# Performance work log

Hardware: AMD Instinct MI355X
Metric: run time of the kernel (lower is better)

Reference implementation:

```python
import jax, jax.numpy as jnp
import numpy as np

V, E, H, L = 32000, 512, 512, 4
B, MAX_LEN = 32, 50
T = MAX_LEN + 1
SOS = 0
PAD_IDX = 2


def setup_inputs() -> dict:
    key = jax.random.key(0)
    ks = jax.random.split(key, 12)
    s = 1.0 / np.sqrt(H)  # pytorch LSTM default init scale
    emb = jax.random.uniform(ks[0], (V, E), minval=-0.1, maxval=0.1)
    emb = emb.at[PAD_IDX].set(0.0)  # padding_idx row zeroed
    inp = {
        "encoder_output": jax.random.normal(ks[1], (B, 50, E), dtype=jnp.float32),
        "decoder_hidden": jax.random.normal(ks[2], (L, B, H), dtype=jnp.float32),
        "decoder_cell": jax.random.normal(ks[3], (L, B, H), dtype=jnp.float32),
        "target_tensor": jax.random.randint(ks[4], (B, T), 0, V),
        "embedding": emb,
        # E == H so all layers stack into one [L, 4H, H] tensor
        "W_ih": jax.random.uniform(ks[5], (L, 4 * H, H), minval=-s, maxval=s),
        "W_hh": jax.random.uniform(ks[6], (L, 4 * H, H), minval=-s, maxval=s),
        "b_ih": jax.random.uniform(ks[7], (L, 4 * H), minval=-s, maxval=s),
        "b_hh": jax.random.uniform(ks[8], (L, 4 * H), minval=-s, maxval=s),
        "W_out": jax.random.uniform(ks[9], (V, H), minval=-0.1, maxval=0.1),
        "b_out": jnp.zeros((V,), dtype=jnp.float32),
    }
    return inp


def reference(encoder_output, decoder_hidden, decoder_cell, target_tensor,
              embedding, W_ih, W_hh, b_ih, b_hh, W_out, b_out):
    # teacher_forcing_ratio == 1 -> input at step 0 is SOS, step i is target[:, i-1]
    bsz = decoder_hidden.shape[1]
    sos = jnp.full((bsz, 1), SOS, dtype=target_tensor.dtype)
    tokens = jnp.concatenate([sos, target_tensor[:, : T - 1]], axis=1)  # [B, T]
    tokens_tb = tokens.T  # [T, B]

    def step(carry, tok):
        h, c = carry  # each [L, B, H]
        x = embedding[tok]  # [B, E]
        new_h, new_c = [], []
        for l in range(L):
            gates = x @ W_ih[l].T + b_ih[l] + h[l] @ W_hh[l].T + b_hh[l]  # [B, 4H]
            i, f, g, o = jnp.split(gates, 4, axis=-1)  # pytorch gate order i,f,g,o
            i, f, o = jax.nn.sigmoid(i), jax.nn.sigmoid(f), jax.nn.sigmoid(o)
            g = jnp.tanh(g)
            c_l = f * c[l] + i * g
            h_l = o * jnp.tanh(c_l)
            new_h.append(h_l)
            new_c.append(c_l)
            x = h_l  # input to next layer (dropout inactive in eval)
        # output projection uses PRE-clamp top-layer hidden (matches torch code)
        logits = x @ W_out.T + b_out  # [B, V]
        h = jnp.clip(jnp.stack(new_h), -50.0, 50.0)
        c = jnp.clip(jnp.stack(new_c), -50.0, 50.0)
        return (h, c), logits

    (h_fin, c_fin), logits_tbv = jax.lax.scan(step, (decoder_hidden, decoder_cell), tokens_tb)
    decoder_outputs = jnp.transpose(logits_tbv, (1, 0, 2))  # [B, T, V]
    return decoder_outputs, h_fin
```

## Files before the change

### kernel.cpp

```cpp
#include <hip/hip_runtime.h>

#define VSZ   32000
#define HSZ   512
#define LSZ   4
#define BSZ   32
#define TSZ   51
#define OUT_LOGITS 52224000
#define MPAD  1664

#define WS_XH    0
#define WS_HTOP  262144
#define WS_WB    688128
#define WS_CNT   8880128

typedef __attribute__((ext_vector_type(8))) short bf16x8;
typedef __attribute__((ext_vector_type(4))) float f32x4;

static __device__ __forceinline__ unsigned short f2bf(float f) {
    unsigned int u = __float_as_uint(f);
    unsigned int r = (u + 0x7FFFu + ((u >> 16) & 1u)) >> 16;
    return (unsigned short)r;
}

static __device__ __forceinline__ void split2(float f0, float f1,
                                              unsigned int& hi, unsigned int& lo) {
    unsigned int u0 = __float_as_uint(f0), u1 = __float_as_uint(f1);
    unsigned int h0 = u0 & 0xffff0000u, h1 = u1 & 0xffff0000u;
    hi = (u0 >> 16) | h1;
    float d0 = f0 - __uint_as_float(h0);
    float d1 = f1 - __uint_as_float(h1);
    lo = (__float_as_uint(d0) >> 16) | (__float_as_uint(d1) & 0xffff0000u);
}

static __device__ __forceinline__ void st_xh(float* p, float v) {
    __hip_atomic_store(p, v, __ATOMIC_RELAXED, __HIP_MEMORY_SCOPE_AGENT);
}
static __device__ __forceinline__ unsigned int ld_cnt(unsigned int* p) {
    return __hip_atomic_load(p, __ATOMIC_RELAXED, __HIP_MEMORY_SCOPE_AGENT);
}

__global__ __launch_bounds__(256) void convw_kernel(const float* __restrict__ W,
                                                    unsigned short* __restrict__ WB) {
    const int n4 = VSZ * HSZ / 4;
    for (int i = blockIdx.x * 256 + threadIdx.x; i < n4; i += gridDim.x * 256) {
        float4 f = ((const float4*)W)[i];
        ushort4 o;
        o.x = f2bf(f.x); o.y = f2bf(f.y); o.z = f2bf(f.z); o.w = f2bf(f.w);
        ((ushort4*)WB)[i] = o;
    }
}

__global__ __launch_bounds__(512, 2) void lstm_kernel(
    const float* __restrict__ dec_h, const float* __restrict__ dec_c,
    const int* __restrict__ target, const float* __restrict__ emb,
    const float* __restrict__ Wih, const float* __restrict__ Whh,
    const float* __restrict__ bih, const float* __restrict__ bhh,
    float* __restrict__ ws, float* __restrict__ out)
{
    __shared__ f32x4 red[4][64];

    float* XH = ws + WS_XH;
    unsigned short* HTOP = (unsigned short*)(ws + WS_HTOP);
    unsigned int* cnt = (unsigned int*)(ws + WS_CNT);

    const int tid  = threadIdx.x;
    const int lane = tid & 63;
    const int w    = tid >> 6;
    const int mt   = (w >> 1) & 1;
    const int nt   = w & 1;
    const int ks   = w >> 2;
    const int mi   = lane & 15;
    const int kg   = lane >> 4;
    const int l    = blockIdx.x >> 6;
    const int jt   = blockIdx.x & 63;

    const int jc = jt * 8 + mt * 4 + kg;
    const int bc = nt * 16 + mi;

    const int rjc = l * 2048 + jc;
    const float bias0 = bih[rjc]        + bhh[rjc];
    const float bias1 = bih[rjc + 512]  + bhh[rjc + 512];
    const float bias2 = bih[rjc + 1024] + bhh[rjc + 1024];
    const float bias3 = bih[rjc + 1536] + bhh[rjc + 1536];

    float c_reg = dec_c[(l * 32 + bc) * 512 + jc];

    bf16x8 wa_hi[16], wa_lo[16];
    {
        const int g_a   = mi & 3;
        const int jl_a  = mt * 4 + (mi >> 2);
        const int row_a = l * 2048 + g_a * 512 + jt * 8 + jl_a;
        const float* wrow = (ks ? Whh : Wih) + (size_t)row_a * 512;
        #pragma unroll
        for (int kk = 0; kk < 16; ++kk) {
            float4 v0 = *(const float4*)(wrow + kk * 32 + kg * 8);
            float4 v1 = *(const float4*)(wrow + kk * 32 + kg * 8 + 4);
            union { unsigned int u[4]; bf16x8 v; } H, L;
            split2(v0.x, v0.y, H.u[0], L.u[0]);
            split2(v0.z, v0.w, H.u[1], L.u[1]);
            split2(v1.x, v1.y, H.u[2], L.u[2]);
            split2(v1.z, v1.w, H.u[3], L.u[3]);
            wa_hi[kk] = H.v; wa_lo[kk] = L.v;
        }
    }

    {
        const int gid = blockIdx.x * 512 + tid;
        if (gid < 16384) {
            int k = gid >> 5, bb = gid & 31;
            st_xh(&XH[131072 + (k >> 2) * 128 + bb * 4 + (k & 3)], emb[k]);
        }
        if (gid < 65536) {
            int l2 = gid >> 14;
            int rem = gid & 16383;
            int j2 = rem >> 5, b2 = rem & 31;
            st_xh(&XH[((l2 + 1) & 1) * 131072 + l2 * 32768 +
                      (128 + (j2 >> 2)) * 128 + b2 * 4 + (j2 & 3)],
                  dec_h[(l2 * 32 + b2) * 512 + j2]);
        }
    }
    __syncthreads();
    if (tid == 0) {
        __builtin_amdgcn_fence(__ATOMIC_RELEASE, "agent");
        __hip_atomic_fetch_add(&cnt[256], 1u, __ATOMIC_RELAXED, __HIP_MEMORY_SCOPE_AGENT);
        while (ld_cnt(&cnt[256]) < 256u) { __builtin_amdgcn_s_sleep(1); }
        __builtin_amdgcn_fence(__ATOMIC_ACQUIRE, "agent");
    }
    __syncthreads();

    for (int s = 0; s < 54; ++s) {
        const int pp = (s + 1) & 1;
        const int pw = s & 1;
        const int t  = s - l;

        if (s > 0 && tid == 0) {
            while (ld_cnt(&cnt[l * 64 + s - 1]) < 64u) {}
            if (l > 0) while (ld_cnt(&cnt[(l - 1) * 64 + s - 1]) < 64u) {}
            if (l < 3) while (ld_cnt(&cnt[(l + 1) * 64 + s - 1]) < 64u) {}
            __builtin_amdgcn_fence(__ATOMIC_ACQUIRE, "agent");
        }
        __syncthreads();

        if (l == 0 && s < 50 && tid < 256) {
            int e = jt * 256 + tid;
            int k = e >> 5, bb = e & 31;
            int tok = target[bb * TSZ + s];
            st_xh(&XH[pw * 131072 + (k >> 2) * 128 + bb * 4 + (k & 3)],
                  emb[tok * 512 + k]);
        }

        if (t >= 0 && t <= 50) {
            const f32x4* xb4 = (const f32x4*)(XH + pp * 131072 + l * 32768)
                               + ks * 4096 + kg * 64 + bc;

            f32x4 acc_a = {0.f, 0.f, 0.f, 0.f};
            f32x4 acc_b = {0.f, 0.f, 0.f, 0.f};
            #pragma unroll
            for (int kk = 0; kk < 16; ++kk) {
                f32x4 x0 = xb4[kk * 256];
                f32x4 x1 = xb4[kk * 256 + 32];
                union { unsigned int u[4]; bf16x8 v; } XHI, XLO;
                split2(x0.x, x0.y, XHI.u[0], XLO.u[0]);
                split2(x0.z, x0.w, XHI.u[1], XLO.u[1]);
                split2(x1.x, x1.y, XHI.u[2], XLO.u[2]);
                split2(x1.z, x1.w, XHI.u[3], XLO.u[3]);
                acc_a = __builtin_amdgcn_mfma_f32_16x16x32_bf16(wa_hi[kk], XHI.v, acc_a, 0, 0, 0);
                acc_b = __builtin_amdgcn_mfma_f32_16x16x32_bf16(wa_lo[kk], XHI.v, acc_b, 0, 0, 0);
                acc_b = __builtin_amdgcn_mfma_f32_16x16x32_bf16(wa_hi[kk], XLO.v, acc_b, 0, 0, 0);
            }
            f32x4 acc = acc_a + acc_b;

            __syncthreads();
            if (w >= 4) red[w - 4][lane] = acc;
            __syncthreads();
            if (w < 4) {
                f32x4 rp = red[w][lane];
                float pi = acc[0] + rp[0] + bias0;
                float pf = acc[1] + rp[1] + bias1;
                float pg = acc[2] + rp[2] + bias2;
                float po = acc[3] + rp[3] + bias3;
                float ig = 1.f / (1.f + expf(-pi));
                float fg = 1.f / (1.f + expf(-pf));
                float gg = tanhf(pg);
                float og = 1.f / (1.f + expf(-po));
                float cn = fg * c_reg + ig * gg;
                float hn = og * tanhf(cn);
                c_reg     = fminf(fmaxf(cn, -50.f), 50.f);
                float hcl = fminf(fmaxf(hn, -50.f), 50.f);

                st_xh(&XH[pw * 131072 + l * 32768 + (128 + (jc >> 2)) * 128 + bc * 4 + (jc & 3)], hcl);
                if (l < 3)
                    st_xh(&XH[pw * 131072 + (l + 1) * 32768 + (jc >> 2) * 128 + bc * 4 + (jc & 3)], hn);
                if (l == 3)
                    HTOP[((t * 32 + bc) << 9) + jc] = f2bf(hn);
                if (t == 50)
                    out[OUT_LOGITS + ((l * 32 + bc) << 9) + jc] = hcl;
            }
        }

        __syncthreads();
        if (tid == 0) {
            __builtin_amdgcn_fence(__ATOMIC_RELEASE, "agent");
            __hip_atomic_fetch_add(&cnt[l * 64 + s], 1u, __ATOMIC_RELAXED,
                                   __HIP_MEMORY_SCOPE_AGENT);
        }
    }
}

__global__ __launch_bounds__(256) void proj_kernel(
    const unsigned short* __restrict__ A, const unsigned short* __restrict__ Bm,
    const float* __restrict__ bout, float* __restrict__ out)
{
    __shared__ unsigned short As[64 * 40];
    __shared__ unsigned short Bs[64 * 40];
    const int tid = threadIdx.x;
    const int bn = blockIdx.x;
    const int bm = blockIdx.y;
    const int w = tid >> 6, lane = tid & 63;
    const int lr = lane & 15, lq = lane >> 4;

    f32x4 acc0 = {0.f, 0.f, 0.f, 0.f};
    f32x4 acc1 = {0.f, 0.f, 0.f, 0.f};
    f32x4 acc2 = {0.f, 0.f, 0.f, 0.f};
    f32x4 acc3 = {0.f, 0.f, 0.f, 0.f};

    const int r = tid >> 2, c8 = (tid & 3) * 8;
    const unsigned short* Ag = A + (bm * 64 + r) * HSZ + c8;
    const unsigned short* Bg = Bm + (size_t)(bn * 64 + r) * HSZ + c8;

    for (int kt = 0; kt < 16; ++kt) {
        *(uint4*)&As[r * 40 + c8] = *(const uint4*)(Ag + kt * 32);
        *(uint4*)&Bs[r * 40 + c8] = *(const uint4*)(Bg + kt * 32);
        __syncthreads();
        bf16x8 af = *(const bf16x8*)&As[(w * 16 + lr) * 40 + lq * 8];
        bf16x8 b0 = *(const bf16x8*)&Bs[(0 * 16 + lr) * 40 + lq * 8];
        bf16x8 b1 = *(const bf16x8*)&Bs[(1 * 16 + lr) * 40 + lq * 8];
        bf16x8 b2 = *(const bf16x8*)&Bs[(2 * 16 + lr) * 40 + lq * 8];
        bf16x8 b3 = *(const bf16x8*)&Bs[(3 * 16 + lr) * 40 + lq * 8];
        acc0 = __builtin_amdgcn_mfma_f32_16x16x32_bf16(af, b0, acc0, 0, 0, 0);
        acc1 = __builtin_amdgcn_mfma_f32_16x16x32_bf16(af, b1, acc1, 0, 0, 0);
        acc2 = __builtin_amdgcn_mfma_f32_16x16x32_bf16(af, b2, acc2, 0, 0, 0);
        acc3 = __builtin_amdgcn_mfma_f32_16x16x32_bf16(af, b3, acc3, 0, 0, 0);
        __syncthreads();
    }

    f32x4 accs[4] = {acc0, acc1, acc2, acc3};
    #pragma unroll
    for (int nt = 0; nt < 4; ++nt) {
        const int v = bn * 64 + nt * 16 + lr;
        const float bo = bout[v];
        #pragma unroll
        for (int reg = 0; reg < 4; ++reg) {
            const int m = bm * 64 + w * 16 + lq * 4 + reg;
            if (m < TSZ * BSZ) {
                const int tt = m >> 5, bb = m & 31;
                out[(size_t)(bb * TSZ + tt) * VSZ + v] = accs[nt][reg] + bo;
            }
        }
    }
}

extern "C" void kernel_launch(void* const* d_in, const int* in_sizes, int n_in,
                              void* d_out, int out_size, void* d_ws, size_t ws_size,
                              hipStream_t stream) {
    const float* dec_h = (const float*)d_in[1];
    const float* dec_c = (const float*)d_in[2];
    const int*   tgt   = (const int*)d_in[3];
    const float* emb   = (const float*)d_in[4];
    const float* Wih   = (const float*)d_in[5];
    const float* Whh   = (const float*)d_in[6];
    const float* bihp  = (const float*)d_in[7];
    const float* bhhp  = (const float*)d_in[8];
    const float* Wout  = (const float*)d_in[9];
    const float* bout  = (const float*)d_in[10];
    float* out = (float*)d_out;
    float* ws  = (float*)d_ws;

    unsigned short* HTOP = (unsigned short*)(ws + WS_HTOP);
    unsigned short* WB   = (unsigned short*)(ws + WS_WB);

    hipMemsetAsync(ws + WS_CNT, 0, 1040, stream);

    convw_kernel<<<4096, 256, 0, stream>>>(Wout, WB);

    void* args[] = { (void*)&dec_h, (void*)&dec_c, (void*)&tgt, (void*)&emb,
                     (void*)&Wih, (void*)&Whh, (void*)&bihp, (void*)&bhhp,
                     (void*)&ws, (void*)&out };
    hipLaunchCooperativeKernel(reinterpret_cast<void*>(lstm_kernel),
                               dim3(256), dim3(512), args, 0, stream);

    proj_kernel<<<dim3(VSZ / 64, MPAD / 64), 256, 0, stream>>>(HTOP, WB, bout, out);
}
```

Baseline: 1.142 ms.

## Store LSTM state pre-split into bf16 hi/lo pairs to skip per-step splitting

```diff
diff --git a/kernel.cpp b/kernel.cpp
--- a/kernel.cpp
+++ b/kernel.cpp
@@ -32,12 +32,21 @@
     lo = (__float_as_uint(d0) >> 16) | (__float_as_uint(d1) & 0xffff0000u);
 }
 
-static __device__ __forceinline__ void st_xh(float* p, float v) {
-    __hip_atomic_store(p, v, __ATOMIC_RELAXED, __HIP_MEMORY_SCOPE_AGENT);
-}
 static __device__ __forceinline__ unsigned int ld_cnt(unsigned int* p) {
     return __hip_atomic_load(p, __ATOMIC_RELAXED, __HIP_MEMORY_SCOPE_AGENT);
 }
+
+static __device__ __forceinline__ void st_split(unsigned short* base, float v) {
+    unsigned int u = __float_as_uint(v);
+    unsigned int h = u & 0xffff0000u;
+    float d = v - __uint_as_float(h);
+    __hip_atomic_store(base, (unsigned short)(u >> 16),
+                       __ATOMIC_RELAXED, __HIP_MEMORY_SCOPE_AGENT);
+    __hip_atomic_store(base + 8, (unsigned short)(__float_as_uint(d) >> 16),
+                       __ATOMIC_RELAXED, __HIP_MEMORY_SCOPE_AGENT);
+}
+
+#define XHB_IDX(buf, layer, k8, b) (((((buf)*4 + (layer))*128 + (k8))*32 + (b))*16)
 
 __global__ __launch_bounds__(256) void convw_kernel(const float* __restrict__ W,
                                                     unsigned short* __restrict__ WB) {
@@ -59,7 +68,7 @@
 {
     __shared__ f32x4 red[4][64];
 
-    float* XH = ws + WS_XH;
+    unsigned short* XHB = (unsigned short*)(ws + WS_XH);
     unsigned short* HTOP = (unsigned short*)(ws + WS_HTOP);
     unsigned int* cnt = (unsigned int*)(ws + WS_CNT);
 
@@ -108,15 +117,14 @@
         const int gid = blockIdx.x * 512 + tid;
         if (gid < 16384) {
             int k = gid >> 5, bb = gid & 31;
-            st_xh(&XH[131072 + (k >> 2) * 128 + bb * 4 + (k & 3)], emb[k]);
+            st_split(XHB + XHB_IDX(1, 0, k >> 3, bb) + (k & 7), emb[k]);
         }
         if (gid < 65536) {
             int l2 = gid >> 14;
             int rem = gid & 16383;
             int j2 = rem >> 5, b2 = rem & 31;
-            st_xh(&XH[((l2 + 1) & 1) * 131072 + l2 * 32768 +
-                      (128 + (j2 >> 2)) * 128 + b2 * 4 + (j2 & 3)],
-                  dec_h[(l2 * 32 + b2) * 512 + j2]);
+            st_split(XHB + XHB_IDX((l2 + 1) & 1, l2, 64 + (j2 >> 3), b2) + (j2 & 7),
+                     dec_h[(l2 * 32 + b2) * 512 + j2]);
         }
     }
     __syncthreads();
@@ -134,9 +142,15 @@
         const int t  = s - l;
 
         if (s > 0 && tid == 0) {
-            while (ld_cnt(&cnt[l * 64 + s - 1]) < 64u) {}
-            if (l > 0) while (ld_cnt(&cnt[(l - 1) * 64 + s - 1]) < 64u) {}
-            if (l < 3) while (ld_cnt(&cnt[(l + 1) * 64 + s - 1]) < 64u) {}
+            unsigned int* c0 = &cnt[l * 64 + s - 1];
+            unsigned int* c1 = (l > 0) ? &cnt[(l - 1) * 64 + s - 1] : c0;
+            unsigned int* c2 = (l < 3) ? &cnt[(l + 1) * 64 + s - 1] : c0;
+            for (;;) {
+                unsigned int a = ld_cnt(c0);
+                unsigned int b2 = ld_cnt(c1);
+                unsigned int c3 = ld_cnt(c2);
+                if (a >= 64u && b2 >= 64u && c3 >= 64u) break;
+            }
             __builtin_amdgcn_fence(__ATOMIC_ACQUIRE, "agent");
         }
         __syncthreads();
@@ -145,32 +159,25 @@
             int e = jt * 256 + tid;
             int k = e >> 5, bb = e & 31;
             int tok = target[bb * TSZ + s];
-            st_xh(&XH[pw * 131072 + (k >> 2) * 128 + bb * 4 + (k & 3)],
-                  emb[tok * 512 + k]);
+            st_split(XHB + XHB_IDX(pw, 0, k >> 3, bb) + (k & 7),
+                     emb[tok * 512 + k]);
         }
 
         if (t >= 0 && t <= 50) {
-            const f32x4* xb4 = (const f32x4*)(XH + pp * 131072 + l * 32768)
-                               + ks * 4096 + kg * 64 + bc;
+            const unsigned short* xb = XHB + XHB_IDX(pp, l, ks * 64 + kg, bc);
 
             f32x4 acc_a = {0.f, 0.f, 0.f, 0.f};
             f32x4 acc_b = {0.f, 0.f, 0.f, 0.f};
             #pragma unroll
             for (int kk = 0; kk < 16; ++kk) {
-                f32x4 x0 = xb4[kk * 256];
-                f32x4 x1 = xb4[kk * 256 + 32];
-                union { unsigned int u[4]; bf16x8 v; } XHI, XLO;
-                split2(x0.x, x0.y, XHI.u[0], XLO.u[0]);
-                split2(x0.z, x0.w, XHI.u[1], XLO.u[1]);
-                split2(x1.x, x1.y, XHI.u[2], XLO.u[2]);
-                split2(x1.z, x1.w, XHI.u[3], XLO.u[3]);
-                acc_a = __builtin_amdgcn_mfma_f32_16x16x32_bf16(wa_hi[kk], XHI.v, acc_a, 0, 0, 0);
-                acc_b = __builtin_amdgcn_mfma_f32_16x16x32_bf16(wa_lo[kk], XHI.v, acc_b, 0, 0, 0);
-                acc_b = __builtin_amdgcn_mfma_f32_16x16x32_bf16(wa_hi[kk], XLO.v, acc_b, 0, 0, 0);
+                bf16x8 xhi = *(const bf16x8*)(xb + kk * 2048);
+                bf16x8 xlo = *(const bf16x8*)(xb + kk * 2048 + 8);
+                acc_a = __builtin_amdgcn_mfma_f32_16x16x32_bf16(wa_hi[kk], xhi, acc_a, 0, 0, 0);
+                acc_b = __builtin_amdgcn_mfma_f32_16x16x32_bf16(wa_lo[kk], xhi, acc_b, 0, 0, 0);
+                acc_b = __builtin_amdgcn_mfma_f32_16x16x32_bf16(wa_hi[kk], xlo, acc_b, 0, 0, 0);
             }
             f32x4 acc = acc_a + acc_b;
 
-            __syncthreads();
             if (w >= 4) red[w - 4][lane] = acc;
             __syncthreads();
             if (w < 4) {
@@ -188,9 +195,9 @@
                 c_reg     = fminf(fmaxf(cn, -50.f), 50.f);
                 float hcl = fminf(fmaxf(hn, -50.f), 50.f);
 
-                st_xh(&XH[pw * 131072 + l * 32768 + (128 + (jc >> 2)) * 128 + bc * 4 + (jc & 3)], hcl);
+                st_split(XHB + XHB_IDX(pw, l, 64 + (jc >> 3), bc) + (jc & 7), hcl);
                 if (l < 3)
-                    st_xh(&XH[pw * 131072 + (l + 1) * 32768 + (jc >> 2) * 128 + bc * 4 + (jc & 3)], hn);
+                    st_split(XHB + XHB_IDX(pw, l + 1, jc >> 3, bc) + (jc & 7), hn);
                 if (l == 3)
                     HTOP[((t * 32 + bc) << 9) + jc] = f2bf(hn);
                 if (t == 50)
```

New measurement: 1.330 ms. 16.5% more time.

## Quad-buffer LSTM state and precompute embeddings to relax inter-layer barriers

Applied to the files above, without the earlier changes.

```diff
diff --git a/kernel.cpp b/kernel.cpp
--- a/kernel.cpp
+++ b/kernel.cpp
@@ -9,9 +9,10 @@
 #define MPAD  1664
 
 #define WS_XH    0
-#define WS_HTOP  262144
-#define WS_WB    688128
-#define WS_CNT   8880128
+#define WS_X0    524288
+#define WS_HTOP  1359872
+#define WS_WB    1785856
+#define WS_CNT   9977856
 
 typedef __attribute__((ext_vector_type(8))) short bf16x8;
 typedef __attribute__((ext_vector_type(4))) float f32x4;
@@ -60,6 +61,7 @@
     __shared__ f32x4 red[4][64];
 
     float* XH = ws + WS_XH;
+    float* X0 = ws + WS_X0;
     unsigned short* HTOP = (unsigned short*)(ws + WS_HTOP);
     unsigned int* cnt = (unsigned int*)(ws + WS_CNT);
 
@@ -106,17 +108,21 @@
 
     {
         const int gid = blockIdx.x * 512 + tid;
-        if (gid < 16384) {
-            int k = gid >> 5, bb = gid & 31;
-            st_xh(&XH[131072 + (k >> 2) * 128 + bb * 4 + (k & 3)], emb[k]);
-        }
         if (gid < 65536) {
             int l2 = gid >> 14;
             int rem = gid & 16383;
             int j2 = rem >> 5, b2 = rem & 31;
-            st_xh(&XH[((l2 + 1) & 1) * 131072 + l2 * 32768 +
+            st_xh(&XH[((l2 + 3) & 3) * 131072 + l2 * 32768 +
                       (128 + (j2 >> 2)) * 128 + b2 * 4 + (j2 & 3)],
                   dec_h[(l2 * 32 + b2) * 512 + j2]);
+        }
+        for (int idx = gid; idx < TSZ * 16384; idx += 131072) {
+            int tt2 = idx >> 14;
+            int rem = idx & 16383;
+            int k = rem >> 5, bb = rem & 31;
+            int tok = tt2 ? target[bb * TSZ + tt2 - 1] : 0;
+            st_xh(&X0[tt2 * 16384 + (k >> 2) * 128 + bb * 4 + (k & 3)],
+                  emb[tok * 512 + k]);
         }
     }
     __syncthreads();
@@ -129,29 +135,29 @@
     __syncthreads();
 
     for (int s = 0; s < 54; ++s) {
-        const int pp = (s + 1) & 1;
-        const int pw = s & 1;
+        const int rp = (s + 3) & 3;
+        const int wp = s & 3;
         const int t  = s - l;
 
         if (s > 0 && tid == 0) {
-            while (ld_cnt(&cnt[l * 64 + s - 1]) < 64u) {}
-            if (l > 0) while (ld_cnt(&cnt[(l - 1) * 64 + s - 1]) < 64u) {}
-            if (l < 3) while (ld_cnt(&cnt[(l + 1) * 64 + s - 1]) < 64u) {}
+            unsigned int* c0 = &cnt[l * 64 + s - 1];
+            unsigned int* c1 = (l > 0) ? &cnt[(l - 1) * 64 + s - 1] : c0;
+            unsigned int* c2 = (l < 3 && s >= 3) ? &cnt[(l + 1) * 64 + s - 3] : c0;
+            for (;;) {
+                unsigned int a  = ld_cnt(c0);
+                unsigned int b2 = ld_cnt(c1);
+                unsigned int c3 = ld_cnt(c2);
+                if (a >= 64u && b2 >= 64u && c3 >= 64u) break;
+            }
             __builtin_amdgcn_fence(__ATOMIC_ACQUIRE, "agent");
         }
         __syncthreads();
 
-        if (l == 0 && s < 50 && tid < 256) {
-            int e = jt * 256 + tid;
-            int k = e >> 5, bb = e & 31;
-            int tok = target[bb * TSZ + s];
-            st_xh(&XH[pw * 131072 + (k >> 2) * 128 + bb * 4 + (k & 3)],
-                  emb[tok * 512 + k]);
-        }
-
         if (t >= 0 && t <= 50) {
-            const f32x4* xb4 = (const f32x4*)(XH + pp * 131072 + l * 32768)
-                               + ks * 4096 + kg * 64 + bc;
+            const float* xbase = (l == 0 && ks == 0)
+                               ? (X0 + t * 16384)
+                               : (XH + rp * 131072 + l * 32768 + ks * 16384);
+            const f32x4* xb4 = (const f32x4*)xbase + kg * 64 + bc;
 
             f32x4 acc_a = {0.f, 0.f, 0.f, 0.f};
             f32x4 acc_b = {0.f, 0.f, 0.f, 0.f};
@@ -170,15 +176,14 @@
             }
             f32x4 acc = acc_a + acc_b;
 
-            __syncthreads();
             if (w >= 4) red[w - 4][lane] = acc;
             __syncthreads();
             if (w < 4) {
-                f32x4 rp = red[w][lane];
-                float pi = acc[0] + rp[0] + bias0;
-                float pf = acc[1] + rp[1] + bias1;
-                float pg = acc[2] + rp[2] + bias2;
-                float po = acc[3] + rp[3] + bias3;
+                f32x4 rp2 = red[w][lane];
+                float pi = acc[0] + rp2[0] + bias0;
+                float pf = acc[1] + rp2[1] + bias1;
+                float pg = acc[2] + rp2[2] + bias2;
+                float po = acc[3] + rp2[3] + bias3;
                 float ig = 1.f / (1.f + expf(-pi));
                 float fg = 1.f / (1.f + expf(-pf));
                 float gg = tanhf(pg);
@@ -188,9 +193,9 @@
                 c_reg     = fminf(fmaxf(cn, -50.f), 50.f);
                 float hcl = fminf(fmaxf(hn, -50.f), 50.f);
 
-                st_xh(&XH[pw * 131072 + l * 32768 + (128 + (jc >> 2)) * 128 + bc * 4 + (jc & 3)], hcl);
+                st_xh(&XH[wp * 131072 + l * 32768 + (128 + (jc >> 2)) * 128 + bc * 4 + (jc & 3)], hcl);
                 if (l < 3)
-                    st_xh(&XH[pw * 131072 + (l + 1) * 32768 + (jc >> 2) * 128 + bc * 4 + (jc & 3)], hn);
+                    st_xh(&XH[wp * 131072 + (l + 1) * 32768 + (jc >> 2) * 128 + bc * 4 + (jc & 3)], hn);
                 if (l == 3)
                     HTOP[((t * 32 + bc) << 9) + jc] = f2bf(hn);
                 if (t == 50)
```

Measured after the change: 1.226 ms. 7.4% more time.
